# Performance work log

Hardware: AMD Instinct MI355X
Metric: run time of the kernel (lower is better)

## Reference

```python
import jax, jax.numpy as jnp
import numpy as np

B, T, D_MODEL, D_HIDDEN, MAX_SEQLEN = 4, 2048, 1024, 1024, 2048


def setup_inputs() -> dict:
    key = jax.random.key(0)
    ks = jax.random.split(key, 8)
    scale = 0.02  # keep exp() and linear outputs in a sane range
    return {
        "q": jax.random.normal(ks[0], (B, T, D_MODEL), dtype=jnp.float32),
        "k": jax.random.normal(ks[1], (B, T, D_MODEL), dtype=jnp.float32),
        "v": jax.random.normal(ks[2], (B, T, D_MODEL), dtype=jnp.float32),
        "Wq": jax.random.normal(ks[3], (D_HIDDEN, D_MODEL), dtype=jnp.float32) * scale,
        "Wk": jax.random.normal(ks[4], (D_HIDDEN, D_MODEL), dtype=jnp.float32) * scale,
        "Wv": jax.random.normal(ks[5], (D_HIDDEN, D_MODEL), dtype=jnp.float32) * scale,
        "Wo": jax.random.normal(ks[6], (D_MODEL, D_HIDDEN), dtype=jnp.float32) * scale,
        "W_bias": jax.random.normal(ks[7], (MAX_SEQLEN, MAX_SEQLEN), dtype=jnp.float32) * scale,
    }


def reference(q, k, v, Wq, Wk, Wv, Wo, W_bias):
    Ti = q.shape[1]
    Tj = k.shape[1]
    # Linear projections (torch Linear: x @ W.T), bias=False
    Q = jnp.einsum('btm,hm->bth', q, Wq)
    K = jnp.einsum('btm,hm->bth', k, Wk)
    V = jnp.einsum('btm,hm->bth', v, Wv)
    pos_bias = W_bias[:Ti, :Tj][None]              # (1, Ti, Tj)
    # Faithful to original: max over dim 0 (batch dim for K, singleton dim for pos_bias)
    max_key = jnp.max(K, axis=0, keepdims=True)    # (1, Tj, Dh)
    max_pos_bias = jnp.max(pos_bias, axis=0, keepdims=True)  # == pos_bias (dim 0 is size 1)
    exp_key = jnp.exp(K - max_key)                 # (B, Tj, Dh)
    exp_pos_bias = jnp.exp(pos_bias - max_pos_bias)  # all-ones, kept for faithfulness
    num = jnp.einsum('bij,bjd->bid', exp_pos_bias, exp_key * V)
    den = jnp.einsum('bij,bjd->bid', exp_pos_bias, exp_key)
    Yt = jax.nn.sigmoid(Q) * num / den             # (B, Ti, Dh)
    return jnp.einsum('bth,mh->btm', Yt, Wo)
```

## Files before the change

kernel.cpp:

```cpp
#include <hip/hip_runtime.h>
#include <hip/hip_bf16.h>

typedef __bf16 bf16;
typedef __bf16 bf16x8 __attribute__((ext_vector_type(8)));
typedef __bf16 bf16x4 __attribute__((ext_vector_type(4)));
typedef float f32x4 __attribute__((ext_vector_type(4)));

#define B_   4
#define T_   2048
#define DM_  1024
#define DH_  1024
#define MROWS 8192

struct CvtJob { const float* src; bf16* dst; int nf4; };
struct CvtArgs { CvtJob job[7]; };

__global__ __launch_bounds__(256) void cvt_kernel(CvtArgs args) {
  CvtJob jb = args.job[blockIdx.y];
  int base = blockIdx.x * 2048;
  if (base >= jb.nf4) return;
  int t2 = threadIdx.x * 2;
  const float4* s = (const float4*)jb.src;
  float4 a[4][2];
#pragma unroll
  for (int u = 0; u < 4; ++u) {
    a[u][0] = s[base + u * 512 + t2];
    a[u][1] = s[base + u * 512 + t2 + 1];
  }
#pragma unroll
  for (int u = 0; u < 4; ++u) {
    bf16x8 o;
    o[0] = (bf16)a[u][0].x; o[1] = (bf16)a[u][0].y;
    o[2] = (bf16)a[u][0].z; o[3] = (bf16)a[u][0].w;
    o[4] = (bf16)a[u][1].x; o[5] = (bf16)a[u][1].y;
    o[6] = (bf16)a[u][1].z; o[7] = (bf16)a[u][1].w;
    *(bf16x8*)(jb.dst + ((size_t)base + u * 512 + t2) * 4) = o;
  }
}

struct GemmJob { const bf16* A; const bf16* Bw; float* Cf; bf16* Cb; int mode; };
struct GemmArgs { GemmJob job[4]; int N; int K; };

__global__ __launch_bounds__(256) void gemm_bt(GemmArgs ga) {
  const GemmJob jb = ga.job[blockIdx.z];
  const int N = ga.N, K = ga.K;
  __shared__ bf16 As[128 * 64];
  __shared__ bf16 Bs[128 * 64];

  const int tid  = threadIdx.x;
  const int lane = tid & 63;
  const int wave = tid >> 6;
  const int wm   = (wave >> 1) * 64;
  const int wn   = (wave & 1) * 64;

  const int f   = blockIdx.y * 8 + blockIdx.x;
  const int xcd = f & 7;
  const int j   = f >> 3;
  const int bn  = j & 7;
  const int bm  = (j >> 3) * 8 + xcd;
  const int tileM = bm * 128;
  const int tileN = bn * 128;

  f32x4 acc[4][4] = {};

  const int sr = lane >> 3;
  const int sc = (lane & 7) ^ sr;

  const char* pa = (const char*)(jb.A  + (size_t)tileM * K);
  const char* pb = (const char*)(jb.Bw + (size_t)tileN * K);
  unsigned int off[4];
#pragma unroll
  for (int l = 0; l < 4; ++l)
    off[l] = (unsigned int)((((wave * 4 + l) * 8 + sr) * K + sc * 8) * 2);

  const int quad = lane >> 4;

  for (int k0 = 0; k0 < K; k0 += 64) {
#pragma unroll
    for (int l = 0; l < 4; ++l) {
      __builtin_amdgcn_global_load_lds(
          (const __attribute__((address_space(1))) void*)(pa + off[l]),
          (__attribute__((address_space(3))) void*)&As[(wave * 4 + l) * 512],
          16, 0, 0);
      __builtin_amdgcn_global_load_lds(
          (const __attribute__((address_space(1))) void*)(pb + off[l]),
          (__attribute__((address_space(3))) void*)&Bs[(wave * 4 + l) * 512],
          16, 0, 0);
    }
    pa += 128;
    pb += 128;
    __syncthreads();

#pragma unroll
    for (int s = 0; s < 2; ++s) {
      bf16x8 af[4], bfr[4];
#pragma unroll
      for (int mt = 0; mt < 4; ++mt) {
        int row = wm + mt * 16 + (lane & 15);
        int chunk = (s * 4 + quad) ^ (row & 7);
        af[mt] = *(const bf16x8*)&As[row * 64 + chunk * 8];
      }
#pragma unroll
      for (int nt = 0; nt < 4; ++nt) {
        int row = wn + nt * 16 + (lane & 15);
        int chunk = (s * 4 + quad) ^ (row & 7);
        bfr[nt] = *(const bf16x8*)&Bs[row * 64 + chunk * 8];
      }
#pragma unroll
      for (int mt = 0; mt < 4; ++mt)
#pragma unroll
        for (int nt = 0; nt < 4; ++nt)
          acc[mt][nt] = __builtin_amdgcn_mfma_f32_16x16x32_bf16(
              af[mt], bfr[nt], acc[mt][nt], 0, 0, 0);
    }
    __syncthreads();
  }

  const int cn = lane & 15;
  const int cr = (lane >> 4) * 4;
  if (jb.mode == 0) {
#pragma unroll
    for (int mt = 0; mt < 4; ++mt)
#pragma unroll
      for (int nt = 0; nt < 4; ++nt)
#pragma unroll
        for (int r = 0; r < 4; ++r) {
          int row = tileM + wm + mt * 16 + cr + r;
          int col = tileN + wn + nt * 16 + cn;
          jb.Cf[(size_t)row * N + col] = acc[mt][nt][r];
        }
  } else if (jb.mode == 1) {
#pragma unroll
    for (int mt = 0; mt < 4; ++mt)
#pragma unroll
      for (int nt = 0; nt < 4; ++nt)
#pragma unroll
        for (int r = 0; r < 4; ++r) {
          int row = tileM + wm + mt * 16 + cr + r;
          int col = tileN + wn + nt * 16 + cn;
          jb.Cb[(size_t)row * N + col] =
              (bf16)(1.f / (1.f + __expf(-acc[mt][nt][r])));
        }
  } else {
#pragma unroll
    for (int mt = 0; mt < 4; ++mt)
#pragma unroll
      for (int nt = 0; nt < 4; ++nt)
#pragma unroll
        for (int r = 0; r < 4; ++r) {
          int row = tileM + wm + mt * 16 + cr + r;
          int col = tileN + wn + nt * 16 + cn;
          jb.Cb[(size_t)row * N + col] = (bf16)acc[mt][nt][r];
        }
  }
}

__global__ __launch_bounds__(256) void reduce_kv(
    const bf16* __restrict__ Kb, const bf16* __restrict__ Vb,
    float* __restrict__ part) {
  __shared__ float lds[64 * 128];
  const int t = threadIdx.x;
  const int half = t >> 7;
  const int dt = t & 127;
  const int d = dt * 8;
  const int j0 = blockIdx.x * 8 + half * 4;
  const size_t bs = (size_t)T_ * DH_;
  float n[4][8] = {}, e[4][8] = {};
  for (int jj = j0; jj < j0 + 4; ++jj) {
    size_t off = (size_t)jj * DH_ + d;
    bf16x8 kk[4], vv[4];
#pragma unroll
    for (int b = 0; b < 4; ++b) {
      kk[b] = *(const bf16x8*)(Kb + off + b * bs);
      vv[b] = *(const bf16x8*)(Vb + off + b * bs);
    }
#pragma unroll
    for (int c = 0; c < 8; ++c) {
      float k0 = (float)kk[0][c], k1 = (float)kk[1][c];
      float k2 = (float)kk[2][c], k3 = (float)kk[3][c];
      float m = fmaxf(fmaxf(k0, k1), fmaxf(k2, k3));
      float w0 = __expf(k0 - m), w1 = __expf(k1 - m);
      float w2 = __expf(k2 - m), w3 = __expf(k3 - m);
      e[0][c] += w0; e[1][c] += w1; e[2][c] += w2; e[3][c] += w3;
      n[0][c] += w0 * (float)vv[0][c];
      n[1][c] += w1 * (float)vv[1][c];
      n[2][c] += w2 * (float)vv[2][c];
      n[3][c] += w3 * (float)vv[3][c];
    }
  }
  if (half) {
#pragma unroll
    for (int b = 0; b < 4; ++b)
#pragma unroll
      for (int c = 0; c < 8; ++c) {
        lds[(b * 8 + c) * 128 + dt] = n[b][c];
        lds[(32 + b * 8 + c) * 128 + dt] = e[b][c];
      }
  }
  __syncthreads();
  if (!half) {
    float* po = part + (size_t)blockIdx.x * 8192;
#pragma unroll
    for (int b = 0; b < 4; ++b)
#pragma unroll
      for (int c = 0; c < 8; ++c) {
        po[b * 1024 + d + c] = n[b][c] + lds[(b * 8 + c) * 128 + dt];
        po[4096 + b * 1024 + d + c] = e[b][c] + lds[(32 + b * 8 + c) * 128 + dt];
      }
  }
}

__global__ __launch_bounds__(256) void finish_kv(
    const float* __restrict__ part, float* __restrict__ numden) {
  __shared__ float lds[128];
  const int t = threadIdx.x;
  const int half = t >> 7;
  const int sl = t & 127;
  const int slot = blockIdx.x * 128 + sl;
  float s = 0.f;
  for (int i = half * 128; i < half * 128 + 128; i += 8) {
#pragma unroll
    for (int u = 0; u < 8; ++u)
      s += part[(size_t)(i + u) * 8192 + slot];
  }
  if (half) lds[sl] = s;
  __syncthreads();
  if (!half) numden[slot] = s + lds[sl];
}

__global__ __launch_bounds__(256) void scale_wo(
    const bf16* __restrict__ Wo, const float* __restrict__ numden,
    bf16* __restrict__ out4) {
  const int b = blockIdx.y;
  size_t i = ((size_t)blockIdx.x * 256 + threadIdx.x) * 8;
  int h = (int)(i & (DH_ - 1));
  bf16x8 w = *(const bf16x8*)(Wo + i);
  const float* nu = numden + b * DH_ + h;
  const float* de = numden + 4096 + b * DH_ + h;
  float4 n0 = *(const float4*)nu;
  float4 n1 = *(const float4*)(nu + 4);
  float4 d0 = *(const float4*)de;
  float4 d1 = *(const float4*)(de + 4);
  bf16x8 o;
  o[0] = (bf16)((float)w[0] * n0.x / d0.x);
  o[1] = (bf16)((float)w[1] * n0.y / d0.y);
  o[2] = (bf16)((float)w[2] * n0.z / d0.z);
  o[3] = (bf16)((float)w[3] * n0.w / d0.w);
  o[4] = (bf16)((float)w[4] * n1.x / d1.x);
  o[5] = (bf16)((float)w[5] * n1.y / d1.y);
  o[6] = (bf16)((float)w[6] * n1.z / d1.z);
  o[7] = (bf16)((float)w[7] * n1.w / d1.w);
  *(bf16x8*)(out4 + (size_t)b * ((size_t)DM_ * DH_) + i) = o;
}

extern "C" void kernel_launch(void* const* d_in, const int* in_sizes, int n_in,
                              void* d_out, int out_size, void* d_ws, size_t ws_size,
                              hipStream_t stream) {
  const float* q  = (const float*)d_in[0];
  const float* k  = (const float*)d_in[1];
  const float* v  = (const float*)d_in[2];
  const float* Wq = (const float*)d_in[3];
  const float* Wk = (const float*)d_in[4];
  const float* Wv = (const float*)d_in[5];
  const float* Wo = (const float*)d_in[6];
  float* out = (float*)d_out;

  char* ws = (char*)d_ws;
  size_t off = 0;
  auto alloc = [&](size_t bytes) {
    char* p = ws + off;
    off += (bytes + 255) & ~(size_t)255;
    return p;
  };
  const size_t actN = (size_t)MROWS * DM_;
  const size_t wN   = (size_t)DH_ * DM_;

  bf16* qb  = (bf16*)alloc(actN * 2);
  bf16* kb  = (bf16*)alloc(actN * 2);
  bf16* vb  = (bf16*)alloc(actN * 2);
  bf16* Wqb = (bf16*)alloc(wN * 2);
  bf16* Wkb = (bf16*)alloc(wN * 2);
  bf16* Wvb = (bf16*)alloc(wN * 2);
  bf16* Wob = (bf16*)alloc(wN * 2);
  bf16* Kb  = (bf16*)alloc(actN * 2);
  bf16* Vb  = (bf16*)alloc(actN * 2);
  bf16* Yb  = (bf16*)alloc(actN * 2);
  float* part = (float*)alloc((size_t)256 * 8192 * 4);
  float* numden = (float*)alloc(8192 * 4);
  bf16* Wob4 = (bf16*)part;

  CvtArgs ca;
  ca.job[0] = {q,  qb,  (int)(actN / 4)};
  ca.job[1] = {k,  kb,  (int)(actN / 4)};
  ca.job[2] = {v,  vb,  (int)(actN / 4)};
  ca.job[3] = {Wq, Wqb, (int)(wN / 4)};
  ca.job[4] = {Wk, Wkb, (int)(wN / 4)};
  ca.job[5] = {Wv, Wvb, (int)(wN / 4)};
  ca.job[6] = {Wo, Wob, (int)(wN / 4)};
  cvt_kernel<<<dim3(actN / 4 / 2048, 7), 256, 0, stream>>>(ca);

  GemmArgs g1;
  g1.N = DH_; g1.K = DM_;
  g1.job[0] = {kb, Wkb, nullptr, Kb, 2};
  g1.job[1] = {vb, Wvb, nullptr, Vb, 2};
  g1.job[2] = {qb, Wqb, nullptr, Yb, 1};
  g1.job[3] = {nullptr, nullptr, nullptr, nullptr, 0};
  gemm_bt<<<dim3(8, MROWS / 128, 3), 256, 0, stream>>>(g1);

  reduce_kv<<<dim3(256), 256, 0, stream>>>(Kb, Vb, part);
  finish_kv<<<dim3(64), 256, 0, stream>>>(part, numden);

  scale_wo<<<dim3(512, 4), 256, 0, stream>>>(Wob, numden, Wob4);

  GemmArgs g2;
  g2.N = DM_; g2.K = DH_;
  for (int b = 0; b < 4; ++b) {
    g2.job[b] = {Yb + (size_t)b * ((size_t)T_ * DH_),
                 Wob4 + (size_t)b * wN,
                 out + (size_t)b * ((size_t)T_ * DM_),
                 nullptr, 0};
  }
  gemm_bt<<<dim3(8, 16, 4), 256, 0, stream>>>(g2);
}
```

Baseline: 278.9 us.

## Switch GEMM to 32x32x16 MFMA and template M-tile size per launch

The bf16 GEMM moves from 16x16x32 MFMA tiles to 32x32x16 MFMA tiles, which reorganises the fragment loads and the output indexing. The M tile becomes a template parameter: 128 rows for the QKV projection and 64 rows for the output projection, whose grid doubles to 8x32x4 to put more blocks in flight. The larger MFMA shape is meant to cut LDS reads and instruction issue per FLOP. The smaller output tile gives more blocks for the smaller GEMM but less reuse of the B tile.

```diff
diff --git a/kernel.cpp b/kernel.cpp
--- a/kernel.cpp
+++ b/kernel.cpp
@@ -5,6 +5,7 @@
 typedef __bf16 bf16x8 __attribute__((ext_vector_type(8)));
 typedef __bf16 bf16x4 __attribute__((ext_vector_type(4)));
 typedef float f32x4 __attribute__((ext_vector_type(4)));
+typedef float f32x16 __attribute__((ext_vector_type(16)));
 
 #define B_   4
 #define T_   2048
@@ -41,16 +42,18 @@
 struct GemmJob { const bf16* A; const bf16* Bw; float* Cf; bf16* Cb; int mode; };
 struct GemmArgs { GemmJob job[4]; int N; int K; };
 
+template <int MT>
 __global__ __launch_bounds__(256) void gemm_bt(GemmArgs ga) {
   const GemmJob jb = ga.job[blockIdx.z];
   const int N = ga.N, K = ga.K;
-  __shared__ bf16 As[128 * 64];
-  __shared__ bf16 Bs[128 * 64];
+  constexpr int TM = MT * 64;
+  __shared__ __align__(16) bf16 As[TM * 64];
+  __shared__ __align__(16) bf16 Bs[128 * 64];
 
   const int tid  = threadIdx.x;
   const int lane = tid & 63;
   const int wave = tid >> 6;
-  const int wm   = (wave >> 1) * 64;
+  const int wm   = (wave >> 1) * (MT * 32);
   const int wn   = (wave & 1) * 64;
 
   const int f   = blockIdx.y * 8 + blockIdx.x;
@@ -58,98 +61,109 @@
   const int j   = f >> 3;
   const int bn  = j & 7;
   const int bm  = (j >> 3) * 8 + xcd;
-  const int tileM = bm * 128;
+  const int tileM = bm * TM;
   const int tileN = bn * 128;
 
-  f32x4 acc[4][4] = {};
+  f32x16 acc[MT][2] = {};
 
   const int sr = lane >> 3;
   const int sc = (lane & 7) ^ sr;
 
   const char* pa = (const char*)(jb.A  + (size_t)tileM * K);
   const char* pb = (const char*)(jb.Bw + (size_t)tileN * K);
-  unsigned int off[4];
+  unsigned int offA[MT * 2], offB[4];
+#pragma unroll
+  for (int l = 0; l < MT * 2; ++l)
+    offA[l] = (unsigned int)((((wave * (MT * 2) + l) * 8 + sr) * K + sc * 8) * 2);
 #pragma unroll
   for (int l = 0; l < 4; ++l)
-    off[l] = (unsigned int)((((wave * 4 + l) * 8 + sr) * K + sc * 8) * 2);
-
-  const int quad = lane >> 4;
+    offB[l] = (unsigned int)((((wave * 4 + l) * 8 + sr) * K + sc * 8) * 2);
+
+  const int half = lane >> 5;
+  const int rc   = lane & 31;
 
   for (int k0 = 0; k0 < K; k0 += 64) {
 #pragma unroll
-    for (int l = 0; l < 4; ++l) {
+    for (int l = 0; l < MT * 2; ++l)
       __builtin_amdgcn_global_load_lds(
-          (const __attribute__((address_space(1))) void*)(pa + off[l]),
-          (__attribute__((address_space(3))) void*)&As[(wave * 4 + l) * 512],
+          (const __attribute__((address_space(1))) void*)(pa + offA[l]),
+          (__attribute__((address_space(3))) void*)&As[(wave * (MT * 2) + l) * 512],
           16, 0, 0);
+#pragma unroll
+    for (int l = 0; l < 4; ++l)
       __builtin_amdgcn_global_load_lds(
-          (const __attribute__((address_space(1))) void*)(pb + off[l]),
+          (const __attribute__((address_space(1))) void*)(pb + offB[l]),
           (__attribute__((address_space(3))) void*)&Bs[(wave * 4 + l) * 512],
           16, 0, 0);
-    }
     pa += 128;
     pb += 128;
     __syncthreads();
 
 #pragma unroll
     for (int s = 0; s < 2; ++s) {
-      bf16x8 af[4], bfr[4];
-#pragma unroll
-      for (int mt = 0; mt < 4; ++mt) {
-        int row = wm + mt * 16 + (lane & 15);
-        int chunk = (s * 4 + quad) ^ (row & 7);
-        af[mt] = *(const bf16x8*)&As[row * 64 + chunk * 8];
-      }
-#pragma unroll
-      for (int nt = 0; nt < 4; ++nt) {
-        int row = wn + nt * 16 + (lane & 15);
-        int chunk = (s * 4 + quad) ^ (row & 7);
-        bfr[nt] = *(const bf16x8*)&Bs[row * 64 + chunk * 8];
-      }
-#pragma unroll
-      for (int mt = 0; mt < 4; ++mt)
-#pragma unroll
-        for (int nt = 0; nt < 4; ++nt)
-          acc[mt][nt] = __builtin_amdgcn_mfma_f32_16x16x32_bf16(
-              af[mt], bfr[nt], acc[mt][nt], 0, 0, 0);
+      bf16x8 af[MT][2], bfr[2][2];
+#pragma unroll
+      for (int mt = 0; mt < MT; ++mt)
+#pragma unroll
+        for (int kk = 0; kk < 2; ++kk) {
+          int row = wm + mt * 32 + rc;
+          int chunk = ((s * 2 + kk) * 2 + half) ^ (row & 7);
+          af[mt][kk] = *(const bf16x8*)&As[row * 64 + chunk * 8];
+        }
+#pragma unroll
+      for (int nt = 0; nt < 2; ++nt)
+#pragma unroll
+        for (int kk = 0; kk < 2; ++kk) {
+          int row = wn + nt * 32 + rc;
+          int chunk = ((s * 2 + kk) * 2 + half) ^ (row & 7);
+          bfr[nt][kk] = *(const bf16x8*)&Bs[row * 64 + chunk * 8];
+        }
+#pragma unroll
+      for (int kk = 0; kk < 2; ++kk)
+#pragma unroll
+        for (int mt = 0; mt < MT; ++mt)
+#pragma unroll
+          for (int nt = 0; nt < 2; ++nt)
+            acc[mt][nt] = __builtin_amdgcn_mfma_f32_32x32x16_bf16(
+                af[mt][kk], bfr[nt][kk], acc[mt][nt], 0, 0, 0);
     }
     __syncthreads();
   }
 
-  const int cn = lane & 15;
-  const int cr = (lane >> 4) * 4;
+  const int cn    = rc;
+  const int rbase = half * 4;
   if (jb.mode == 0) {
 #pragma unroll
-    for (int mt = 0; mt < 4; ++mt)
-#pragma unroll
-      for (int nt = 0; nt < 4; ++nt)
-#pragma unroll
-        for (int r = 0; r < 4; ++r) {
-          int row = tileM + wm + mt * 16 + cr + r;
-          int col = tileN + wn + nt * 16 + cn;
+    for (int mt = 0; mt < MT; ++mt)
+#pragma unroll
+      for (int nt = 0; nt < 2; ++nt)
+#pragma unroll
+        for (int r = 0; r < 16; ++r) {
+          int row = tileM + wm + mt * 32 + rbase + (r & 3) + 8 * (r >> 2);
+          int col = tileN + wn + nt * 32 + cn;
           jb.Cf[(size_t)row * N + col] = acc[mt][nt][r];
         }
   } else if (jb.mode == 1) {
 #pragma unroll
-    for (int mt = 0; mt < 4; ++mt)
-#pragma unroll
-      for (int nt = 0; nt < 4; ++nt)
-#pragma unroll
-        for (int r = 0; r < 4; ++r) {
-          int row = tileM + wm + mt * 16 + cr + r;
-          int col = tileN + wn + nt * 16 + cn;
+    for (int mt = 0; mt < MT; ++mt)
+#pragma unroll
+      for (int nt = 0; nt < 2; ++nt)
+#pragma unroll
+        for (int r = 0; r < 16; ++r) {
+          int row = tileM + wm + mt * 32 + rbase + (r & 3) + 8 * (r >> 2);
+          int col = tileN + wn + nt * 32 + cn;
           jb.Cb[(size_t)row * N + col] =
               (bf16)(1.f / (1.f + __expf(-acc[mt][nt][r])));
         }
   } else {
 #pragma unroll
-    for (int mt = 0; mt < 4; ++mt)
-#pragma unroll
-      for (int nt = 0; nt < 4; ++nt)
-#pragma unroll
-        for (int r = 0; r < 4; ++r) {
-          int row = tileM + wm + mt * 16 + cr + r;
-          int col = tileN + wn + nt * 16 + cn;
+    for (int mt = 0; mt < MT; ++mt)
+#pragma unroll
+      for (int nt = 0; nt < 2; ++nt)
+#pragma unroll
+        for (int r = 0; r < 16; ++r) {
+          int row = tileM + wm + mt * 32 + rbase + (r & 3) + 8 * (r >> 2);
+          int col = tileN + wn + nt * 32 + cn;
           jb.Cb[(size_t)row * N + col] = (bf16)acc[mt][nt][r];
         }
   }
@@ -305,7 +319,7 @@
   g1.job[1] = {vb, Wvb, nullptr, Vb, 2};
   g1.job[2] = {qb, Wqb, nullptr, Yb, 1};
   g1.job[3] = {nullptr, nullptr, nullptr, nullptr, 0};
-  gemm_bt<<<dim3(8, MROWS / 128, 3), 256, 0, stream>>>(g1);
+  gemm_bt<2><<<dim3(8, MROWS / 128, 3), 256, 0, stream>>>(g1);
 
   reduce_kv<<<dim3(256), 256, 0, stream>>>(Kb, Vb, part);
   finish_kv<<<dim3(64), 256, 0, stream>>>(part, numden);
@@ -320,5 +334,5 @@
                  out + (size_t)b * ((size_t)T_ * DM_),
                  nullptr, 0};
   }
-  gemm_bt<<<dim3(8, 16, 4), 256, 0, stream>>>(g2);
-}
+  gemm_bt<1><<<dim3(8, 32, 4), 256, 0, stream>>>(g2);
+}
```

New measurement: 274.3 us. Within noise of the previous version (-1.7%).
